# Kernel tuning notes

Hardware: AMD Instinct MI355X
Metric: run time of the kernel (lower is better)

## Reference

```python
import jax, jax.numpy as jnp
import numpy as np

PI = np.pi
B, N, H, W = 32, 200000, 1024, 2048


def cloud2idx(xyz):
    # xyz: (B, N, 3) -> equirectangular grid coords in [-1, 1], shape (B, N, 2)
    theta = jnp.arctan2(jnp.linalg.norm(xyz[..., :2], axis=-1), xyz[..., 2])  # polar angle in [0, pi]
    phi = jnp.arctan2(xyz[..., 1], xyz[..., 0]) + PI                          # azimuth in [0, 2*pi]
    u = 1.0 - phi / (2.0 * PI)   # horizontal image coord in [0, 1]
    v = theta / PI               # vertical image coord in [0, 1]
    return jnp.stack([2.0 * u - 1.0, 2.0 * v - 1.0], axis=-1)


def sample_from_img(img, coord):
    # Bilinear grid_sample, align_corners=False, zeros padding.
    # img: (H, W, C); coord: (B, N, 2) in [-1, 1] (x, y order) -> (B, N, C)
    h, w = img.shape[0], img.shape[1]
    x = (coord[..., 0] + 1.0) * (w * 0.5) - 0.5
    y = (coord[..., 1] + 1.0) * (h * 0.5) - 0.5
    x0 = jnp.floor(x)
    y0 = jnp.floor(y)
    wx = x - x0
    wy = y - y0

    def gather(xi, yi):
        valid = (xi >= 0) & (xi <= w - 1) & (yi >= 0) & (yi <= h - 1)
        xc = jnp.clip(xi, 0, w - 1).astype(jnp.int32)
        yc = jnp.clip(yi, 0, h - 1).astype(jnp.int32)
        return img[yc, xc] * valid[..., None].astype(img.dtype)

    return (gather(x0, y0) * ((1.0 - wx) * (1.0 - wy))[..., None]
            + gather(x0 + 1.0, y0) * (wx * (1.0 - wy))[..., None]
            + gather(x0, y0 + 1.0) * ((1.0 - wx) * wy)[..., None]
            + gather(x0 + 1.0, y0 + 1.0) * (wx * wy)[..., None])


def setup_inputs() -> dict:
    key = jax.random.key(0)
    ks = jax.random.split(key, 7)
    return {
        "xyz": jax.random.normal(ks[0], (1, N, 3), jnp.float32) * 2.0,
        "rgb": jax.random.uniform(ks[1], (1, N, 3), jnp.float32),
        "img": jax.random.uniform(ks[2], (H, W, 3), jnp.float32),
        "translation": jax.random.normal(ks[3], (B, 3, 1), jnp.float32) * 0.1,
        "yaw": jax.random.uniform(ks[4], (B, 1), jnp.float32) * (2.0 * PI),
        "pitch": jax.random.uniform(ks[5], (B, 1), jnp.float32) * PI,
        "roll": jax.random.uniform(ks[6], (B, 1), jnp.float32) * PI,
    }


def _forward(xyz, rgb, img, translation, yaw, pitch, roll):
    z = jnp.zeros_like(yaw)
    o = jnp.ones_like(yaw)  # (B, 1)
    cr, sr = jnp.cos(roll), jnp.sin(roll)
    cp, sp = jnp.cos(pitch), jnp.sin(pitch)
    cy, sy = jnp.cos(yaw), jnp.sin(yaw)
    # (B, 3, 3) rotation matrices, same row layout as the torch code
    RX = jnp.concatenate([jnp.stack([o, z, z], -1),
                          jnp.stack([z, cr, -sr], -1),
                          jnp.stack([z, sr, cr], -1)], axis=1)
    RY = jnp.concatenate([jnp.stack([cp, z, sp], -1),
                          jnp.stack([z, o, z], -1),
                          jnp.stack([-sp, z, cp], -1)], axis=1)
    RZ = jnp.concatenate([jnp.stack([cy, -sy, z], -1),
                          jnp.stack([sy, cy, z], -1),
                          jnp.stack([z, z, o], -1)], axis=1)
    Rm = RZ @ RY @ RX  # (B, 3, 3)

    new_xyz = xyz - jnp.swapaxes(translation, 1, 2)       # (1,N,3) - (B,1,3) -> (B,N,3)
    new_xyz = jnp.einsum('bij,bnj->bni', Rm, new_xyz)      # rotate each point by row-dot

    coord = cloud2idx(new_xyz)                             # (B, N, 2)
    sample_rgb = sample_from_img(img, coord)               # (B, N, 3)

    mask = jnp.sum(sample_rgb == 0, axis=-1) != 3          # (B, N) bool
    per_pt = jnp.linalg.norm(sample_rgb - rgb, axis=-1) * mask.astype(sample_rgb.dtype)
    rgb_loss_list = per_pt.sum(-1) / mask.sum(-1).astype(per_pt.dtype)  # (B,)
    return rgb_loss_list


def reference(xyz, rgb, img, translation, yaw, pitch, roll):
    rgb_loss_list = _forward(xyz, rgb, img, translation, yaw, pitch, roll)
    return (rgb_loss_list.sum(), rgb_loss_list)
```

## Files before the change

### kernel.cpp

```cpp
#include <hip/hip_runtime.h>
#include <math.h>
#include <stdint.h>

#define PI_F 3.14159265358979323846f
#define HALF_PI_F 1.57079632679489662f

#define IMG_H 1024
#define IMG_W 2048
#define NB 8


__device__ __forceinline__ float fast_atan2f(float y, float x) {
    float ax = fabsf(x), ay = fabsf(y);
    float mx = fmaxf(ax, ay), mn = fminf(ax, ay);
    float a = __fdividef(mn, mx);
    float s = a * a;
    float r = fmaf(s, -0.01172120f, 0.05265332f);
    r = fmaf(s, r, -0.11643287f);
    r = fmaf(s, r, 0.19354346f);
    r = fmaf(s, r, -0.33262347f);
    r = fmaf(s, r, 0.99997726f);
    r = r * a;
    if (ay > ax) r = HALF_PI_F - r;
    if (x < 0.0f) r = PI_F - r;
    return copysignf(r, y);
}

__device__ __forceinline__ float dec_r(uint32_t t) { return (float)((t >> 11) & 31u) * (1.0f / 31.0f); }
__device__ __forceinline__ float dec_g(uint32_t t) { return (float)((t >> 5) & 63u) * (1.0f / 63.0f); }
__device__ __forceinline__ float dec_b(uint32_t t) { return (float)(t & 31u) * (1.0f / 31.0f); }

__device__ __forceinline__ uint32_t quant565(const float* __restrict__ img, size_t pix) {
    float r = img[pix + 0], g = img[pix + 1], b = img[pix + 2];
    uint32_t r5 = min((uint32_t)__float2uint_rn(r * 31.0f), 31u);
    uint32_t g6 = min((uint32_t)__float2uint_rn(g * 63.0f), 63u);
    uint32_t b5 = min((uint32_t)__float2uint_rn(b * 31.0f), 31u);
    return (r5 << 11) | (g6 << 5) | b5;
}

__global__ __launch_bounds__(256) void bsl_pack_setup(
        const float* __restrict__ img, uint32_t* __restrict__ vp,
        const float* __restrict__ yaw, const float* __restrict__ pitch,
        const float* __restrict__ roll, float* __restrict__ rm,
        float* __restrict__ sums, float* __restrict__ cnts, int B) {
    if (blockIdx.x == 0 && threadIdx.x < 32) {
        int b = threadIdx.x;
        if (b < B) {
            float cr = cosf(roll[b]),  sr = sinf(roll[b]);
            float cp = cosf(pitch[b]), sp = sinf(pitch[b]);
            float cy = cosf(yaw[b]),   sy = sinf(yaw[b]);
            float RX[9] = {1.f, 0.f, 0.f,   0.f, cr, -sr,   0.f, sr,  cr};
            float RY[9] = {cp,  0.f, sp,    0.f, 1.f, 0.f,  -sp, 0.f, cp};
            float RZ[9] = {cy, -sy, 0.f,    sy,  cy, 0.f,   0.f, 0.f, 1.f};
            float A[9], M[9];
            for (int i = 0; i < 3; ++i)
                for (int j = 0; j < 3; ++j) {
                    float s = 0.f;
                    for (int k = 0; k < 3; ++k) s += RZ[i*3+k] * RY[k*3+j];
                    A[i*3+j] = s;
                }
            for (int i = 0; i < 3; ++i)
                for (int j = 0; j < 3; ++j) {
                    float s = 0.f;
                    for (int k = 0; k < 3; ++k) s += A[i*3+k] * RX[k*3+j];
                    M[i*3+j] = s;
                }
            for (int k = 0; k < 9; ++k) rm[b*9+k] = M[k];
            sums[b] = 0.f;
            cnts[b] = 0.f;
        }
    }
    int idx = blockIdx.x * 256 + threadIdx.x;
    if (idx < IMG_H * IMG_W) {
        int y = idx >> 11;
        int x = idx & (IMG_W - 1);
        int y1 = min(y + 1, IMG_H - 1);
        uint32_t lo = quant565(img, (size_t)idx * 3);
        uint32_t hi = quant565(img, ((size_t)y1 * IMG_W + x) * 3);
        vp[idx] = lo | (hi << 16);
    }
}

__global__ __launch_bounds__(256) void bsl_main(
        const float* __restrict__ xyz,
        const float* __restrict__ rgb,
        const uint32_t* __restrict__ vp,
        const float* __restrict__ trans,
        const float* __restrict__ rm,
        float* __restrict__ sums,
        float* __restrict__ cnts,
        int n_pts) {
    const int b0 = blockIdx.y * NB;
    const int tid = threadIdx.x;
    const int n = blockIdx.x * 256 + tid;

    float accs[NB], cnl[NB];
    #pragma unroll
    for (int nb = 0; nb < NB; ++nb) { accs[nb] = 0.f; cnl[nb] = 0.f; }

    if (n < n_pts) {
        float px = __builtin_nontemporal_load(&xyz[3*n+0]);
        float py = __builtin_nontemporal_load(&xyz[3*n+1]);
        float pz = __builtin_nontemporal_load(&xyz[3*n+2]);
        float r0 = __builtin_nontemporal_load(&rgb[3*n+0]);
        float r1 = __builtin_nontemporal_load(&rgb[3*n+1]);
        float r2 = __builtin_nontemporal_load(&rgb[3*n+2]);

        #pragma unroll
        for (int nb = 0; nb < NB; ++nb) {
            const int b = b0 + nb;
            const float* R = rm + b * 9;
            const float* T = trans + b * 3;
            float qx = px - T[0], qy = py - T[1], qz = pz - T[2];

            float vx = R[0]*qx + R[1]*qy + R[2]*qz;
            float vy = R[3]*qx + R[4]*qy + R[5]*qz;
            float vz = R[6]*qx + R[7]*qy + R[8]*qz;

            float rxy   = sqrtf(vx*vx + vy*vy);
            float theta = fast_atan2f(rxy, vz);
            float praw  = fast_atan2f(vy, vx);

            float xf = fmaf(praw,  -325.949323452f, 1023.5f);
            float yf = fmaf(theta,  325.949323452f, -0.5f);

            float x0f = floorf(xf), y0f = floorf(yf);
            float wx = xf - x0f, wy = yf - y0f;
            int x0 = (int)x0f, y0 = (int)y0f;
            int x1 = x0 + 1, y1 = y0 + 1;

            bool vx0 = (x0 >= 0) & (x0 <= IMG_W - 1);
            bool vx1 = (x1 >= 0) & (x1 <= IMG_W - 1);
            bool vy0 = (y0 >= 0) & (y0 <= IMG_H - 1);
            bool vy1 = (y1 >= 0) & (y1 <= IMG_H - 1);
            float w00 = (vx0 & vy0) ? (1.0f - wx) * (1.0f - wy) : 0.0f;
            float w10 = (vx1 & vy0) ? wx * (1.0f - wy) : 0.0f;
            float w01 = (vx0 & vy1) ? (1.0f - wx) * wy : 0.0f;
            float w11 = (vx1 & vy1) ? wx * wy : 0.0f;

            int x0c = min(max(x0, 0), IMG_W - 1);
            int x1c = min(max(x1, 0), IMG_W - 1);
            int y0c = min(max(y0, 0), IMG_H - 1);
            int y1c = min(max(y1, 0), IMG_H - 1);
            bool sy = (y1c != y0c);

            uint32_t wA = vp[(size_t)y0c * IMG_W + x0c];
            uint32_t wB = vp[(size_t)y0c * IMG_W + x1c];
            uint32_t t00 = wA & 0xffffu;
            uint32_t t10 = wB & 0xffffu;
            uint32_t t01 = sy ? (wA >> 16) : t00;
            uint32_t t11 = sy ? (wB >> 16) : t10;

            float s0 = dec_r(t00)*w00 + dec_r(t10)*w10 + dec_r(t01)*w01 + dec_r(t11)*w11;
            float s1 = dec_g(t00)*w00 + dec_g(t10)*w10 + dec_g(t01)*w01 + dec_g(t11)*w11;
            float s2 = dec_b(t00)*w00 + dec_b(t10)*w10 + dec_b(t01)*w01 + dec_b(t11)*w11;

            bool m = !((s0 == 0.0f) && (s1 == 0.0f) && (s2 == 0.0f));

            float d0 = s0 - r0;
            float d1 = s1 - r1;
            float d2 = s2 - r2;
            float per = sqrtf(d0*d0 + d1*d1 + d2*d2);

            accs[nb] += m ? per : 0.0f;
            cnl[nb]  += m ? 1.0f : 0.0f;
        }
    }

    __shared__ float lsum[4][NB], lcnt[4][NB];
    int wid = tid >> 6;
    int lane = tid & 63;
    #pragma unroll
    for (int nb = 0; nb < NB; ++nb) {
        float a = accs[nb], c = cnl[nb];
        #pragma unroll
        for (int off = 32; off > 0; off >>= 1) {
            a += __shfl_down(a, off, 64);
            c += __shfl_down(c, off, 64);
        }
        if (lane == 0) { lsum[wid][nb] = a; lcnt[wid][nb] = c; }
    }
    __syncthreads();
    if (tid < NB * 2) {
        int nb = tid & (NB - 1);
        int k = tid >> 3;
        float v = 0.f;
        #pragma unroll
        for (int w = 0; w < 4; ++w) v += k ? lcnt[w][nb] : lsum[w][nb];
        atomicAdd(k ? &cnts[b0 + nb] : &sums[b0 + nb], v);
    }
}

__global__ void bsl_finalize(const float* __restrict__ sums,
                             const float* __restrict__ cnts,
                             float* __restrict__ out,
                             int B) {
    int b = threadIdx.x;
    float loss = 0.f;
    if (b < B) {
        loss = sums[b] / cnts[b];
        out[1 + b] = loss;
    }
    #pragma unroll
    for (int off = 32; off > 0; off >>= 1)
        loss += __shfl_down(loss, off, 64);
    if (b == 0) out[0] = loss;
}

extern "C" void kernel_launch(void* const* d_in, const int* in_sizes, int n_in,
                              void* d_out, int out_size, void* d_ws, size_t ws_size,
                              hipStream_t stream) {
    const float* xyz   = (const float*)d_in[0];
    const float* rgb   = (const float*)d_in[1];
    const float* img   = (const float*)d_in[2];
    const float* trans = (const float*)d_in[3];
    const float* yaw   = (const float*)d_in[4];
    const float* pitch = (const float*)d_in[5];
    const float* roll  = (const float*)d_in[6];
    float* out = (float*)d_out;

    const int n_pts = in_sizes[0] / 3;
    const int B     = in_sizes[3] / 3;

    float* ws   = (float*)d_ws;
    float* rm   = ws;
    float* sums = ws + 9 * B;
    float* cnts = ws + 10 * B;
    uint32_t* vp = (uint32_t*)((char*)d_ws + 2048);

    bsl_pack_setup<<<(IMG_H * IMG_W + 255) / 256, 256, 0, stream>>>(
        img, vp, yaw, pitch, roll, rm, sums, cnts, B);

    dim3 grid((n_pts + 255) / 256, B / NB);
    bsl_main<<<grid, 256, 0, stream>>>(xyz, rgb, vp, trans, rm, sums, cnts, n_pts);

    bsl_finalize<<<1, 64, 0, stream>>>(sums, cnts, out, B);
}
```

Measured before the change: 157.5 us.

## Sort points into direction bins before sampling to improve gather locality

Adds a histogram, scan and scatter pass that buckets points by their untransformed spherical direction (128x64 bins) and writes interleaved xyz+rgb records in bucket order. The main kernel then reads these sorted records, so neighbouring threads in a wavefront are meant to land on nearby image texels after rotation, improving cache hit rates on the random gathers. The packed image layout also changes from overlapping row pairs to disjoint row pairs, which needs four gathers per sample instead of two. The trade-off is three extra launches, atomics on the histogram, a single-block scan, a 4.8 MB scatter write, and the doubled gather count.

After: 176.9 us. 12.3% more time.

```diff
diff --git a/kernel.cpp b/kernel.cpp
--- a/kernel.cpp
+++ b/kernel.cpp
@@ -8,7 +8,13 @@
 #define IMG_H 1024
 #define IMG_W 2048
 #define NB 8
-
+#define NBINS_T 128
+#define NBINS_P 64
+#define NBINS (NBINS_T * NBINS_P)
+
+#define HIST_OFF  2048
+#define PK_OFF    65536
+#define PTS_OFF   (65536 + 4 * 1024 * 1024)
 
 __device__ __forceinline__ float fast_atan2f(float y, float x) {
     float ax = fabsf(x), ay = fabsf(y);
@@ -26,11 +32,15 @@
     return copysignf(r, y);
 }
 
-__device__ __forceinline__ float dec_r(uint32_t t) { return (float)((t >> 11) & 31u) * (1.0f / 31.0f); }
-__device__ __forceinline__ float dec_g(uint32_t t) { return (float)((t >> 5) & 63u) * (1.0f / 63.0f); }
-__device__ __forceinline__ float dec_b(uint32_t t) { return (float)(t & 31u) * (1.0f / 31.0f); }
-
-__device__ __forceinline__ uint32_t quant565(const float* __restrict__ img, size_t pix) {
+__device__ __forceinline__ int dir_key(float x, float y, float z) {
+    float theta = fast_atan2f(sqrtf(x * x + y * y), z);
+    float phi   = fast_atan2f(y, x);
+    int tb = min(max((int)(theta * ((float)NBINS_T / PI_F)), 0), NBINS_T - 1);
+    int pb = min(max((int)((phi + PI_F) * ((float)NBINS_P / (2.0f * PI_F))), 0), NBINS_P - 1);
+    return tb * NBINS_P + pb;
+}
+
+__device__ __forceinline__ uint32_t quant565(const float* __restrict__ img, int pix) {
     float r = img[pix + 0], g = img[pix + 1], b = img[pix + 2];
     uint32_t r5 = min((uint32_t)__float2uint_rn(r * 31.0f), 31u);
     uint32_t g6 = min((uint32_t)__float2uint_rn(g * 63.0f), 63u);
@@ -38,13 +48,26 @@
     return (r5 << 11) | (g6 << 5) | b5;
 }
 
-__global__ __launch_bounds__(256) void bsl_pack_setup(
-        const float* __restrict__ img, uint32_t* __restrict__ vp,
+__global__ __launch_bounds__(256) void bsl_pack_hist(
+        const float* __restrict__ img, uint32_t* __restrict__ pk,
+        const float* __restrict__ xyz, uint32_t* __restrict__ hist,
         const float* __restrict__ yaw, const float* __restrict__ pitch,
         const float* __restrict__ roll, float* __restrict__ rm,
-        float* __restrict__ sums, float* __restrict__ cnts, int B) {
-    if (blockIdx.x == 0 && threadIdx.x < 32) {
-        int b = threadIdx.x;
+        float* __restrict__ sums, float* __restrict__ cnts,
+        int B, int n_pts) {
+    const int bx = blockIdx.x;
+    const int tid = threadIdx.x;
+    if (bx < 4096) {
+        int idx = bx * 256 + tid;
+        int p = idx >> 11;
+        int x = idx & (IMG_W - 1);
+        uint32_t lo = quant565(img, ((2 * p) * IMG_W + x) * 3);
+        uint32_t hi = quant565(img, ((2 * p + 1) * IMG_W + x) * 3);
+        pk[idx] = lo | (hi << 16);
+        return;
+    }
+    if (bx == 4096 && tid < 32) {
+        int b = tid;
         if (b < B) {
             float cr = cosf(roll[b]),  sr = sinf(roll[b]);
             float cp = cosf(pitch[b]), sp = sinf(pitch[b]);
@@ -70,21 +93,49 @@
             cnts[b] = 0.f;
         }
     }
-    int idx = blockIdx.x * 256 + threadIdx.x;
-    if (idx < IMG_H * IMG_W) {
-        int y = idx >> 11;
-        int x = idx & (IMG_W - 1);
-        int y1 = min(y + 1, IMG_H - 1);
-        uint32_t lo = quant565(img, (size_t)idx * 3);
-        uint32_t hi = quant565(img, ((size_t)y1 * IMG_W + x) * 3);
-        vp[idx] = lo | (hi << 16);
-    }
+    int n = (bx - 4096) * 256 + tid;
+    if (n < n_pts) {
+        int k = dir_key(xyz[3*n+0], xyz[3*n+1], xyz[3*n+2]);
+        atomicAdd(&hist[k], 1u);
+    }
+}
+
+__global__ __launch_bounds__(256) void bsl_scan(uint32_t* __restrict__ hist) {
+    __shared__ uint32_t part[256];
+    int t = threadIdx.x;
+    uint32_t local[32];
+    uint32_t s = 0;
+    #pragma unroll
+    for (int i = 0; i < 32; ++i) { local[i] = hist[t * 32 + i]; s += local[i]; }
+    part[t] = s;
+    __syncthreads();
+    for (int off = 1; off < 256; off <<= 1) {
+        uint32_t v = (t >= off) ? part[t - off] : 0u;
+        __syncthreads();
+        part[t] += v;
+        __syncthreads();
+    }
+    uint32_t run = (t == 0) ? 0u : part[t - 1];
+    #pragma unroll
+    for (int i = 0; i < 32; ++i) { uint32_t c = local[i]; hist[t * 32 + i] = run; run += c; }
+}
+
+__global__ __launch_bounds__(256) void bsl_scatter(
+        const float* __restrict__ xyz, const float* __restrict__ rgb,
+        uint32_t* __restrict__ hist, float* __restrict__ pts, int n_pts) {
+    int n = blockIdx.x * 256 + threadIdx.x;
+    if (n >= n_pts) return;
+    float x = xyz[3*n+0], y = xyz[3*n+1], z = xyz[3*n+2];
+    int k = dir_key(x, y, z);
+    uint32_t pos = atomicAdd(&hist[k], 1u);
+    float* p = pts + (size_t)pos * 6;
+    p[0] = x; p[1] = y; p[2] = z;
+    p[3] = rgb[3*n+0]; p[4] = rgb[3*n+1]; p[5] = rgb[3*n+2];
 }
 
 __global__ __launch_bounds__(256) void bsl_main(
-        const float* __restrict__ xyz,
-        const float* __restrict__ rgb,
-        const uint32_t* __restrict__ vp,
+        const float* __restrict__ pts,
+        const uint32_t* __restrict__ pk,
         const float* __restrict__ trans,
         const float* __restrict__ rm,
         float* __restrict__ sums,
@@ -99,12 +150,13 @@
     for (int nb = 0; nb < NB; ++nb) { accs[nb] = 0.f; cnl[nb] = 0.f; }
 
     if (n < n_pts) {
-        float px = __builtin_nontemporal_load(&xyz[3*n+0]);
-        float py = __builtin_nontemporal_load(&xyz[3*n+1]);
-        float pz = __builtin_nontemporal_load(&xyz[3*n+2]);
-        float r0 = __builtin_nontemporal_load(&rgb[3*n+0]);
-        float r1 = __builtin_nontemporal_load(&rgb[3*n+1]);
-        float r2 = __builtin_nontemporal_load(&rgb[3*n+2]);
+        const float* P = pts + (size_t)n * 6;
+        float px = __builtin_nontemporal_load(&P[0]);
+        float py = __builtin_nontemporal_load(&P[1]);
+        float pz = __builtin_nontemporal_load(&P[2]);
+        float r0 = __builtin_nontemporal_load(&P[3]);
+        float r1 = __builtin_nontemporal_load(&P[4]);
+        float r2 = __builtin_nontemporal_load(&P[5]);
 
         #pragma unroll
         for (int nb = 0; nb < NB; ++nb) {
@@ -142,18 +194,24 @@
             int x1c = min(max(x1, 0), IMG_W - 1);
             int y0c = min(max(y0, 0), IMG_H - 1);
             int y1c = min(max(y1, 0), IMG_H - 1);
-            bool sy = (y1c != y0c);
-
-            uint32_t wA = vp[(size_t)y0c * IMG_W + x0c];
-            uint32_t wB = vp[(size_t)y0c * IMG_W + x1c];
-            uint32_t t00 = wA & 0xffffu;
-            uint32_t t10 = wB & 0xffffu;
-            uint32_t t01 = sy ? (wA >> 16) : t00;
-            uint32_t t11 = sy ? (wB >> 16) : t10;
-
-            float s0 = dec_r(t00)*w00 + dec_r(t10)*w10 + dec_r(t01)*w01 + dec_r(t11)*w11;
-            float s1 = dec_g(t00)*w00 + dec_g(t10)*w10 + dec_g(t01)*w01 + dec_g(t11)*w11;
-            float s2 = dec_b(t00)*w00 + dec_b(t10)*w10 + dec_b(t01)*w01 + dec_b(t11)*w11;
+
+            uint32_t rowA = ((uint32_t)(y0c >> 1)) << 11;
+            uint32_t rowB = ((uint32_t)(y1c >> 1)) << 11;
+            uint32_t wA = pk[rowA + (uint32_t)x0c];
+            uint32_t wB = pk[rowA + (uint32_t)x1c];
+            uint32_t wC = pk[rowB + (uint32_t)x0c];
+            uint32_t wD = pk[rowB + (uint32_t)x1c];
+            uint32_t t00 = (y0c & 1) ? (wA >> 16) : (wA & 0xffffu);
+            uint32_t t10 = (y0c & 1) ? (wB >> 16) : (wB & 0xffffu);
+            uint32_t t01 = (y1c & 1) ? (wC >> 16) : (wC & 0xffffu);
+            uint32_t t11 = (y1c & 1) ? (wD >> 16) : (wD & 0xffffu);
+
+            float s0 = (float)(t00 >> 11) * (1.0f/31.0f) * w00 + (float)(t10 >> 11) * (1.0f/31.0f) * w10
+                     + (float)(t01 >> 11) * (1.0f/31.0f) * w01 + (float)(t11 >> 11) * (1.0f/31.0f) * w11;
+            float s1 = (float)((t00 >> 5) & 63u) * (1.0f/63.0f) * w00 + (float)((t10 >> 5) & 63u) * (1.0f/63.0f) * w10
+                     + (float)((t01 >> 5) & 63u) * (1.0f/63.0f) * w01 + (float)((t11 >> 5) & 63u) * (1.0f/63.0f) * w11;
+            float s2 = (float)(t00 & 31u) * (1.0f/31.0f) * w00 + (float)(t10 & 31u) * (1.0f/31.0f) * w10
+                     + (float)(t01 & 31u) * (1.0f/31.0f) * w01 + (float)(t11 & 31u) * (1.0f/31.0f) * w11;
 
             bool m = !((s0 == 0.0f) && (s1 == 0.0f) && (s2 == 0.0f));
 
@@ -222,17 +280,26 @@
     const int n_pts = in_sizes[0] / 3;
     const int B     = in_sizes[3] / 3;
 
-    float* ws   = (float*)d_ws;
-    float* rm   = ws;
-    float* sums = ws + 9 * B;
-    float* cnts = ws + 10 * B;
-    uint32_t* vp = (uint32_t*)((char*)d_ws + 2048);
-
-    bsl_pack_setup<<<(IMG_H * IMG_W + 255) / 256, 256, 0, stream>>>(
-        img, vp, yaw, pitch, roll, rm, sums, cnts, B);
-
-    dim3 grid((n_pts + 255) / 256, B / NB);
-    bsl_main<<<grid, 256, 0, stream>>>(xyz, rgb, vp, trans, rm, sums, cnts, n_pts);
+    float* ws    = (float*)d_ws;
+    float* rm    = ws;
+    float* sums  = ws + 9 * B;
+    float* cnts  = ws + 10 * B;
+    uint32_t* hist = (uint32_t*)((char*)d_ws + HIST_OFF);
+    uint32_t* pk   = (uint32_t*)((char*)d_ws + PK_OFF);
+    float*    pts  = (float*)((char*)d_ws + PTS_OFF);
+
+    hipMemsetAsync(hist, 0, NBINS * sizeof(uint32_t), stream);
+
+    const int key_blocks = (n_pts + 255) / 256;
+    bsl_pack_hist<<<4096 + key_blocks, 256, 0, stream>>>(
+        img, pk, xyz, hist, yaw, pitch, roll, rm, sums, cnts, B, n_pts);
+
+    bsl_scan<<<1, 256, 0, stream>>>(hist);
+
+    bsl_scatter<<<key_blocks, 256, 0, stream>>>(xyz, rgb, hist, pts, n_pts);
+
+    dim3 grid(key_blocks, B / NB);
+    bsl_main<<<grid, 256, 0, stream>>>(pts, pk, trans, rm, sums, cnts, n_pts);
 
     bsl_finalize<<<1, 64, 0, stream>>>(sums, cnts, out, B);
 }
```
